# Kernel optimization log

Measured on AMD Instinct MI355X. Metric: run time of the kernel, lower is better.

Reference implementation:

```python
import jax, jax.numpy as jnp
import numpy as np

DIM = 1024
HEADS = 16
HEAD_DIM = DIM // HEADS
MLP_HIDDEN = DIM * 4
EPS = 1e-6


def _ln(x):
    # LayerNorm without affine, eps=1e-6
    mu = jnp.mean(x, axis=-1, keepdims=True)
    var = jnp.var(x, axis=-1, keepdims=True)
    return (x - mu) / jnp.sqrt(var + EPS)


def setup_inputs() -> dict:
    key = jax.random.key(0)
    ks = jax.random.split(key, 12)
    B, N = 8, 1024
    s = lambda fan: 1.0 / np.sqrt(fan)
    return {
        "x": jax.random.normal(ks[0], (B, N, DIM), jnp.float32),
        "c": jax.random.normal(ks[1], (B, DIM), jnp.float32),
        "w_qkv": jax.random.normal(ks[2], (DIM, 3 * DIM), jnp.float32) * s(DIM),
        "b_qkv": jnp.zeros((3 * DIM,), jnp.float32),
        "w_proj": jax.random.normal(ks[3], (DIM, DIM), jnp.float32) * s(DIM),
        "b_proj": jnp.zeros((DIM,), jnp.float32),
        "w_mlp1": jax.random.normal(ks[4], (DIM, MLP_HIDDEN), jnp.float32) * s(DIM),
        "b_mlp1": jnp.zeros((MLP_HIDDEN,), jnp.float32),
        "w_mlp2": jax.random.normal(ks[5], (MLP_HIDDEN, DIM), jnp.float32) * s(MLP_HIDDEN),
        "b_mlp2": jnp.zeros((DIM,), jnp.float32),
        "w_ada": jax.random.normal(ks[6], (DIM, 6 * DIM), jnp.float32) * s(DIM),
        "b_ada": jnp.zeros((6 * DIM,), jnp.float32),
    }


def _attention(h, w_qkv, b_qkv, w_proj, b_proj):
    B, N, C = h.shape
    qkv = h @ w_qkv + b_qkv  # [B,N,3C]
    qkv = qkv.reshape(B, N, 3, HEADS, HEAD_DIM)
    q, k, v = qkv[:, :, 0], qkv[:, :, 1], qkv[:, :, 2]  # [B,N,H,Dh]
    scale = HEAD_DIM ** -0.5
    attn = jnp.einsum("bqhd,bkhd->bhqk", q, k) * scale
    attn = jax.nn.softmax(attn, axis=-1)
    o = jnp.einsum("bhqk,bkhd->bqhd", attn, v).reshape(B, N, C)
    return o @ w_proj + b_proj


def reference(x, c, w_qkv, b_qkv, w_proj, b_proj, w_mlp1, b_mlp1, w_mlp2, b_mlp2, w_ada, b_ada):
    mod = (jax.nn.silu(c) @ w_ada + b_ada)[:, None, :]  # [B,1,6D]
    g1, be1, a1, g2, be2, a2 = jnp.split(mod, 6, axis=-1)
    h = _ln(x) * (1.0 + g1) + be1
    x = x + a1 * _attention(h, w_qkv, b_qkv, w_proj, b_proj)
    h = _ln(x) * (1.0 + g2) + be2
    mlp = jax.nn.gelu(h @ w_mlp1 + b_mlp1, approximate=False) @ w_mlp2 + b_mlp2
    return x + a2 * mlp
```

## Files before the change

kernel.cpp:

```cpp
#include <hip/hip_runtime.h>
#include <hip/hip_bf16.h>

#define DIMC 1024
#define SEQ  1024
#define NB   8
#define NH   16
#define HD2  64
#define EPSV 1e-6f

typedef short short8 __attribute__((ext_vector_type(8)));
typedef float floatx4 __attribute__((ext_vector_type(4)));

#define GLOAD_LDS(g, l) \
  __builtin_amdgcn_global_load_lds((const __attribute__((address_space(1))) unsigned int*)(g), \
                                   (__attribute__((address_space(3))) unsigned int*)(l), 16, 0, 0)

__device__ __forceinline__ float bf2f(unsigned short u){
  union { float f; unsigned int i; } v; v.i = ((unsigned int)u) << 16; return v.f;
}
__device__ __forceinline__ unsigned short f2bf(float f){
  union { float f; unsigned int i; } v; v.f = f;
  unsigned int r = v.i + 0x7fffu + ((v.i >> 16) & 1u);
  return (unsigned short)(r >> 16);
}

__global__ __launch_bounds__(256)
void tcvt_kernel(const float* __restrict__ in, unsigned short* __restrict__ out, int K, int N)
{
  __shared__ float tile[32][33];
  const int n0 = blockIdx.x * 32;
  const int k0 = blockIdx.y * 32;
  const int tx = threadIdx.x & 31;
  const int ty = threadIdx.x >> 5;
#pragma unroll
  for (int i = 0; i < 4; i++)
    tile[ty + i*8][tx] = in[(size_t)(k0 + ty + i*8) * N + n0 + tx];
  __syncthreads();
#pragma unroll
  for (int i = 0; i < 4; i++)
    out[(size_t)(n0 + ty + i*8) * K + k0 + tx] = f2bf(tile[tx][ty + i*8]);
}

__global__ __launch_bounds__(256)
void ada1_kernel(const float* __restrict__ c,
                 const float* __restrict__ w_ada,
                 float* __restrict__ partial)
{
  __shared__ float cs[NB][128];
  const int chunk = blockIdx.y;
  const int col = blockIdx.x * 256 + threadIdx.x;
  const int t = threadIdx.x;
  for (int i = t; i < NB * 128; i += 256) {
    const int b = i >> 7, k = i & 127;
    const float v = c[b * DIMC + chunk * 128 + k];
    cs[b][k] = v / (1.0f + __expf(-v));
  }
  __syncthreads();
  float acc[NB];
#pragma unroll
  for (int b = 0; b < NB; b++) acc[b] = 0.0f;
#pragma unroll 8
  for (int k = 0; k < 128; k++) {
    const float wv = w_ada[(size_t)(chunk * 128 + k) * 6144 + col];
#pragma unroll
    for (int b = 0; b < NB; b++) acc[b] = fmaf(cs[b][k], wv, acc[b]);
  }
#pragma unroll
  for (int b = 0; b < NB; b++)
    partial[((size_t)chunk * NB + b) * 6144 + col] = acc[b];
}

__global__ __launch_bounds__(256)
void ada2_kernel(const float* __restrict__ partial, const float* __restrict__ b_ada,
                 float* __restrict__ mod)
{
  const int i = blockIdx.x * 256 + threadIdx.x;
  const int b = i / 6144, col = i % 6144;
  float s = b_ada[col];
#pragma unroll
  for (int ch = 0; ch < 8; ch++) s += partial[((size_t)ch * NB + b) * 6144 + col];
  mod[i] = s;
}

__global__ __launch_bounds__(256)
void ln_kernel(const float* __restrict__ xin, const float* __restrict__ mod,
               int goff, int boff, unsigned short* __restrict__ hout)
{
  const int row = blockIdx.x;
  const int bb = row >> 10;
  const int t = threadIdx.x;
  const float4 x4 = *((const float4*)(xin + (size_t)row * DIMC) + t);
  const float v0 = x4.x, v1 = x4.y, v2 = x4.z, v3 = x4.w;
  float s  = v0 + v1 + v2 + v3;
  float ss = v0*v0 + v1*v1 + v2*v2 + v3*v3;
#pragma unroll
  for (int off = 32; off > 0; off >>= 1) {
    s  += __shfl_down(s,  off, 64);
    ss += __shfl_down(ss, off, 64);
  }
  __shared__ float red[10];
  const int w = t >> 6;
  if ((t & 63) == 0) { red[w] = s; red[4 + w] = ss; }
  __syncthreads();
  if (t == 0) {
    const float S  = red[0] + red[1] + red[2] + red[3];
    const float SS = red[4] + red[5] + red[6] + red[7];
    const float mu = S * (1.0f / 1024.0f);
    red[8] = mu;
    red[9] = rsqrtf(SS * (1.0f / 1024.0f) - mu * mu + EPSV);
  }
  __syncthreads();
  const float mu = red[8], rstd = red[9];
  const float* mrow = mod + (size_t)bb * 6144;
  const int d = t * 4;
  const float h0 = (v0 - mu) * rstd * (1.0f + mrow[goff + d + 0]) + mrow[boff + d + 0];
  const float h1 = (v1 - mu) * rstd * (1.0f + mrow[goff + d + 1]) + mrow[boff + d + 1];
  const float h2 = (v2 - mu) * rstd * (1.0f + mrow[goff + d + 2]) + mrow[boff + d + 2];
  const float h3 = (v3 - mu) * rstd * (1.0f + mrow[goff + d + 3]) + mrow[boff + d + 3];
  uint2 u;
  u.x = (unsigned)f2bf(h0) | ((unsigned)f2bf(h1) << 16);
  u.y = (unsigned)f2bf(h2) | ((unsigned)f2bf(h3) << 16);
  *((uint2*)(hout + (size_t)row * DIMC + d)) = u;
}

#define MF(a, b, c) __builtin_amdgcn_mfma_f32_16x16x32_bf16(a, b, c, 0, 0, 0)
#define FENCE() asm volatile("" ::: "memory")
#define BARRIER() do { FENCE(); __builtin_amdgcn_s_barrier(); FENCE(); } while (0)

template<int MODE>
__global__ __launch_bounds__(512, 2)
void gemm256_kernel(const unsigned short* __restrict__ A,
                    const unsigned short* __restrict__ Bt,
                    const float* __restrict__ bias,
                    void* __restrict__ Cout,
                    const float* __restrict__ resid,
                    const float* __restrict__ mod,
                    int M, int N, int K)
{
  __shared__ unsigned short As[2][16384];
  __shared__ unsigned short Bs[2][16384];

  const int mT = M >> 8;
  const int mb = mT >> 3;
  const int bid = blockIdx.x;
  const int xcd = bid & 7;
  const int local = bid >> 3;
  const int ni = local / mb;
  const int mi = xcd * mb + (local - ni * mb);
  const int m0 = mi << 8, n0 = ni << 8;

  const int tid = threadIdx.x;
  const int w = tid >> 6, lane = tid & 63;
  const int quad = lane >> 4, c16 = lane & 15;
  const int wm = w >> 2, wn = w & 3, w2 = w << 1;

  const int aRow = wm * 8192 + c16 * 64;
  const int bRow = (wn >> 1) * 8192 + ((wn & 1) * 64 + c16) * 64;
  const int sxz  = (c16 & 7) << 4;
  const int swz0 = ((0  + quad * 16) ^ sxz) >> 1;
  const int swz1 = ((64 + quad * 16) ^ sxz) >> 1;
#define LDA8(cc, i, SW) (*(const short8*)&As[cc][aRow + (i) * 1024 + (SW)])
#define LDB8(cc, j, SW) (*(const short8*)&Bs[cc][bRow + (j) * 1024 + (SW)])

  const int l8 = lane >> 3, lc = lane & 7;
  const int stC = ((lc ^ l8) << 3);
  const unsigned short* aSt = A  + (size_t)(m0 + w2 * 8 + l8) * K + stC;
  const unsigned short* bSt = Bt + (size_t)(n0 + w2 * 8 + l8) * K + stC;
#define STAGE_A(cc, h, kk0) do { \
  GLOAD_LDS(aSt + (size_t)((h) * 128    ) * K + (kk0), &As[cc][(h) * 8192 + w2 * 512      ]); \
  GLOAD_LDS(aSt + (size_t)((h) * 128 + 8) * K + (kk0), &As[cc][(h) * 8192 + w2 * 512 + 512]); \
} while (0)
#define STAGE_B(cc, h, kk0) do { \
  GLOAD_LDS(bSt + (size_t)((h) * 128    ) * K + (kk0), &Bs[cc][(h) * 8192 + w2 * 512      ]); \
  GLOAD_LDS(bSt + (size_t)((h) * 128 + 8) * K + (kk0), &Bs[cc][(h) * 8192 + w2 * 512 + 512]); \
} while (0)

  floatx4 acc[8][4];
#pragma unroll
  for (int i = 0; i < 8; i++)
#pragma unroll
    for (int j = 0; j < 4; j++) acc[i][j] = (floatx4)(0.0f);

#define MMROW(i, aE, aO) do { \
  acc[i][0] = MF(aE, bF00, acc[i][0]); acc[i][0] = MF(aO, bF01, acc[i][0]); \
  acc[i][1] = MF(aE, bF10, acc[i][1]); acc[i][1] = MF(aO, bF11, acc[i][1]); \
  acc[i][2] = MF(aE, bF20, acc[i][2]); acc[i][2] = MF(aO, bF21, acc[i][2]); \
  acc[i][3] = MF(aE, bF30, acc[i][3]); acc[i][3] = MF(aO, bF31, acc[i][3]); \
} while (0)

#define PH_TAIL(i0, i1) do { \
  BARRIER(); \
  asm volatile("s_waitcnt lgkmcnt(0)" ::: "memory"); \
  __builtin_amdgcn_s_setprio(1); \
  MMROW(i0, a0, a1); \
  MMROW(i1, a2, a3); \
  __builtin_amdgcn_s_setprio(0); \
} while (0)

#define GROUP(cc, oo, g) do { \
  const int kA_ = ((g) + 1) << 6; const int kB_ = ((g) + 2) << 6; \
  const bool dA_ = kA_ < K; const bool dB_ = kB_ < K; \
  short8 bF00 = LDB8(cc, 0, swz0), bF01 = LDB8(cc, 0, swz1); \
  short8 bF10 = LDB8(cc, 1, swz0), bF11 = LDB8(cc, 1, swz1); \
  short8 bF20 = LDB8(cc, 2, swz0), bF21 = LDB8(cc, 2, swz1); \
  short8 bF30 = LDB8(cc, 3, swz0), bF31 = LDB8(cc, 3, swz1); \
  short8 a0 = LDA8(cc, 0, swz0), a1 = LDA8(cc, 0, swz1); \
  short8 a2 = LDA8(cc, 1, swz0), a3 = LDA8(cc, 1, swz1); \
  if (dA_) STAGE_A(oo, 0, kA_); \
  PH_TAIL(0, 1); \
  BARRIER(); \
  a0 = LDA8(cc, 2, swz0); a1 = LDA8(cc, 2, swz1); \
  a2 = LDA8(cc, 3, swz0); a3 = LDA8(cc, 3, swz1); \
  if (dA_) STAGE_A(oo, 1, kA_); \
  PH_TAIL(2, 3); \
  BARRIER(); \
  a0 = LDA8(cc, 4, swz0); a1 = LDA8(cc, 4, swz1); \
  a2 = LDA8(cc, 5, swz0); a3 = LDA8(cc, 5, swz1); \
  if (dB_) STAGE_B(cc, 0, kB_); \
  PH_TAIL(4, 5); \
  BARRIER(); \
  a0 = LDA8(cc, 6, swz0); a1 = LDA8(cc, 6, swz1); \
  a2 = LDA8(cc, 7, swz0); a3 = LDA8(cc, 7, swz1); \
  if (dB_) STAGE_B(cc, 1, kB_); \
  PH_TAIL(6, 7); \
  if (dB_) { asm volatile("s_waitcnt vmcnt(4)" ::: "memory"); } \
  else     { asm volatile("s_waitcnt vmcnt(0)" ::: "memory"); } \
  BARRIER(); \
} while (0)

  STAGE_B(0, 0, 0);  STAGE_B(0, 1, 0);
  STAGE_A(0, 0, 0);  STAGE_A(0, 1, 0);
  STAGE_B(1, 0, 64); STAGE_B(1, 1, 64);
  asm volatile("s_waitcnt vmcnt(4)" ::: "memory");
  BARRIER();

  const int T = K >> 6;
  for (int g = 0; g < T; g += 2) {
    GROUP(0, 1, g);
    GROUP(1, 0, g + 1);
  }

  const int bb = m0 >> 10;
#pragma unroll
  for (int j = 0; j < 4; j++) {
    const int col = n0 + wn * 64 + j * 16 + c16;
    const float bv = bias[col];
    float av = 0.0f;
    if (MODE == 2) av = mod[(size_t)bb * 6144 + 2048 + col];
    if (MODE == 3) av = mod[(size_t)bb * 6144 + 5120 + col];
#pragma unroll
    for (int i = 0; i < 8; i++) {
      const int rowb = m0 + wm * 128 + i * 16 + quad * 4;
#pragma unroll
      for (int r = 0; r < 4; r++) {
        const int row = rowb + r;
        const size_t idx = (size_t)row * N + col;
        float v = acc[i][j][r] + bv;
        if (MODE == 0) {
          ((unsigned short*)Cout)[idx] = f2bf(v);
        } else if (MODE == 1) {
          v = 0.5f * v * (1.0f + erff(v * 0.70710678f));
          ((unsigned short*)Cout)[idx] = f2bf(v);
        } else {
          ((float*)Cout)[idx] = fmaf(av, v, resid[idx]);
        }
      }
    }
  }
#undef GROUP
#undef PH_TAIL
#undef MMROW
#undef STAGE_A
#undef STAGE_B
#undef LDA8
#undef LDB8
}

__global__ __launch_bounds__(256, 2)
void fattn_kernel(const unsigned short* __restrict__ qkv, unsigned short* __restrict__ o_out)
{
  __shared__ unsigned short Ks[64][72];
  __shared__ unsigned short Vt[64][72];
  __shared__ unsigned short Pt[4][32][72];

  const int blk = blockIdx.x;
  const int qt = blk & 7;
  const int h  = (blk >> 3) & 15;
  const int bb = blk >> 7;
  const int tid = threadIdx.x;
  const int w = tid >> 6;
  const int lane = tid & 63;
  const int quad = lane >> 4;
  const int c16 = lane & 15;
  const int q0 = qt * 128 + w * 32;

  short8 qf[2][2];
#pragma unroll
  for (int msub = 0; msub < 2; msub++)
#pragma unroll
    for (int kh = 0; kh < 2; kh++) {
      const size_t idx = ((size_t)((bb*SEQ + q0 + msub*16 + c16) * 3 + 0)) * DIMC
                       + h * HD2 + kh * 32 + quad * 8;
      const uint4 u = *(const uint4*)(qkv + idx);
      const unsigned short* pu = (const unsigned short*)&u;
      short8 r;
#pragma unroll
      for (int j = 0; j < 8; j++) r[j] = (short)f2bf(bf2f(pu[j]) * 0.125f);
      qf[msub][kh] = r;
    }

  floatx4 oacc[2][4];
  float lsum[2][4];
#pragma unroll
  for (int msub = 0; msub < 2; msub++) {
#pragma unroll
    for (int r = 0; r < 4; r++) lsum[msub][r] = 0.0f;
#pragma unroll
    for (int d = 0; d < 4; d++) oacc[msub][d] = (floatx4)(0.0f);
  }

  const int tok = tid & 63;
  const int dg = tid >> 6;

  for (int kt = 0; kt < 16; kt++) {
    __syncthreads();
    {
      const size_t base = ((size_t)((bb*SEQ + kt*64 + tok) * 3)) * DIMC + h * HD2 + dg * 16;
      const uint4 ku0 = *(const uint4*)(qkv + base + DIMC);
      const uint4 ku1 = *(const uint4*)(qkv + base + DIMC + 8);
      const uint4 vu0 = *(const uint4*)(qkv + base + 2*DIMC);
      const uint4 vu1 = *(const uint4*)(qkv + base + 2*DIMC + 8);
      *(uint4*)&Ks[tok][dg*16]     = ku0;
      *(uint4*)&Ks[tok][dg*16 + 8] = ku1;
      const unsigned short* vp0 = (const unsigned short*)&vu0;
      const unsigned short* vp1 = (const unsigned short*)&vu1;
#pragma unroll
      for (int j = 0; j < 8; j++) Vt[dg*16 + j][tok] = vp0[j];
#pragma unroll
      for (int j = 0; j < 8; j++) Vt[dg*16 + 8 + j][tok] = vp1[j];
    }
    __syncthreads();

    floatx4 s[2][4];
#pragma unroll
    for (int msub = 0; msub < 2; msub++)
#pragma unroll
      for (int nsub = 0; nsub < 4; nsub++) s[msub][nsub] = (floatx4)(0.0f);
#pragma unroll
    for (int nsub = 0; nsub < 4; nsub++) {
      const short8 kf0 = *(const short8*)&Ks[nsub*16 + c16][quad*8];
      const short8 kf1 = *(const short8*)&Ks[nsub*16 + c16][32 + quad*8];
#pragma unroll
      for (int msub = 0; msub < 2; msub++) {
        s[msub][nsub] = __builtin_amdgcn_mfma_f32_16x16x32_bf16(qf[msub][0], kf0, s[msub][nsub], 0, 0, 0);
        s[msub][nsub] = __builtin_amdgcn_mfma_f32_16x16x32_bf16(qf[msub][1], kf1, s[msub][nsub], 0, 0, 0);
      }
    }

#pragma unroll
    for (int msub = 0; msub < 2; msub++)
#pragma unroll
      for (int nsub = 0; nsub < 4; nsub++)
#pragma unroll
        for (int r = 0; r < 4; r++) {
          const float p = __expf(s[msub][nsub][r] - 8.0f);
          lsum[msub][r] += p;
          Pt[w][msub*16 + quad*4 + r][nsub*16 + c16] = f2bf(p);
        }

    short8 pa[2][2];
#pragma unroll
    for (int msub = 0; msub < 2; msub++) {
      pa[msub][0] = *(const short8*)&Pt[w][msub*16 + c16][quad*8];
      pa[msub][1] = *(const short8*)&Pt[w][msub*16 + c16][32 + quad*8];
    }
#pragma unroll
    for (int dsub = 0; dsub < 4; dsub++) {
      const short8 vf0 = *(const short8*)&Vt[dsub*16 + c16][quad*8];
      const short8 vf1 = *(const short8*)&Vt[dsub*16 + c16][32 + quad*8];
#pragma unroll
      for (int msub = 0; msub < 2; msub++) {
        oacc[msub][dsub] = __builtin_amdgcn_mfma_f32_16x16x32_bf16(pa[msub][0], vf0, oacc[msub][dsub], 0, 0, 0);
        oacc[msub][dsub] = __builtin_amdgcn_mfma_f32_16x16x32_bf16(pa[msub][1], vf1, oacc[msub][dsub], 0, 0, 0);
      }
    }
  }

#pragma unroll
  for (int msub = 0; msub < 2; msub++) {
    float rl[4];
#pragma unroll
    for (int r = 0; r < 4; r++) {
      float t = lsum[msub][r];
#pragma unroll
      for (int xm = 1; xm < 16; xm <<= 1) t += __shfl_xor(t, xm, 64);
      rl[r] = 1.0f / t;
    }
#pragma unroll
    for (int dsub = 0; dsub < 4; dsub++)
#pragma unroll
      for (int r = 0; r < 4; r++) {
        const size_t idx = (size_t)(bb*SEQ + q0 + msub*16 + quad*4 + r) * DIMC
                         + h * HD2 + dsub*16 + c16;
        o_out[idx] = f2bf(oacc[msub][dsub][r] * rl[r]);
      }
  }
}

extern "C" void kernel_launch(void* const* d_in, const int* in_sizes, int n_in,
                              void* d_out, int out_size, void* d_ws, size_t ws_size,
                              hipStream_t stream) {
  const float* x      = (const float*)d_in[0];
  const float* c      = (const float*)d_in[1];
  const float* w_qkv  = (const float*)d_in[2];
  const float* b_qkv  = (const float*)d_in[3];
  const float* w_proj = (const float*)d_in[4];
  const float* b_proj = (const float*)d_in[5];
  const float* w_mlp1 = (const float*)d_in[6];
  const float* b_mlp1 = (const float*)d_in[7];
  const float* w_mlp2 = (const float*)d_in[8];
  const float* b_mlp2 = (const float*)d_in[9];
  const float* w_ada  = (const float*)d_in[10];
  const float* b_ada  = (const float*)d_in[11];

  char* ws = (char*)d_ws;
  float*          mod     = (float*)(ws);
  unsigned short* wqkv_t  = (unsigned short*)(ws + 196608);
  unsigned short* wproj_t = (unsigned short*)(ws + 6488064);
  unsigned short* wmlp1_t = (unsigned short*)(ws + 8585216);
  unsigned short* wmlp2_t = (unsigned short*)(ws + 16973824);
  unsigned short* bufH    = (unsigned short*)(ws + 25362432);
  float*          adapart = (float*)(ws + 25362432);
  unsigned short* qkv     = (unsigned short*)(ws + 42139648);
  unsigned short* hid     = (unsigned short*)(ws + 42139648);
  float*          out     = (float*)d_out;

  const int M = NB * SEQ;

  tcvt_kernel<<<dim3(96, 32),  256, 0, stream>>>(w_qkv,  wqkv_t,  1024, 3072);
  tcvt_kernel<<<dim3(32, 32),  256, 0, stream>>>(w_proj, wproj_t, 1024, 1024);
  tcvt_kernel<<<dim3(128, 32), 256, 0, stream>>>(w_mlp1, wmlp1_t, 1024, 4096);
  tcvt_kernel<<<dim3(32, 128), 256, 0, stream>>>(w_mlp2, wmlp2_t, 4096, 1024);

  ada1_kernel<<<dim3(24, 8), 256, 0, stream>>>(c, w_ada, adapart);
  ada2_kernel<<<192, 256, 0, stream>>>(adapart, b_ada, mod);

  ln_kernel<<<M, 256, 0, stream>>>(x, mod, 0, 1024, bufH);
  gemm256_kernel<0><<<384, 512, 0, stream>>>(bufH, wqkv_t, b_qkv, qkv, nullptr, nullptr, M, 3072, 1024);
  fattn_kernel<<<1024, 256, 0, stream>>>(qkv, bufH);
  gemm256_kernel<2><<<128, 512, 0, stream>>>(bufH, wproj_t, b_proj, out, x, mod, M, 1024, 1024);
  ln_kernel<<<M, 256, 0, stream>>>(out, mod, 3072, 4096, bufH);

  const size_t fullHidEnd = 42139648ull + (size_t)M * 4096 * 2;
  if (ws_size >= fullHidEnd) {
    gemm256_kernel<1><<<512, 512, 0, stream>>>(bufH, wmlp1_t, b_mlp1, hid,
                                               nullptr, nullptr, M, 4096, 1024);
    gemm256_kernel<3><<<128, 512, 0, stream>>>(hid, wmlp2_t, b_mlp2, out,
                                               out, mod, M, 1024, 4096);
  } else {
    for (int half = 0; half < 2; half++) {
      const size_t roff = (size_t)half * 4096;
      gemm256_kernel<1><<<256, 512, 0, stream>>>(bufH + roff * DIMC, wmlp1_t, b_mlp1, hid,
                                                 nullptr, nullptr, 4096, 4096, 1024);
      gemm256_kernel<3><<<64, 512, 0, stream>>>(hid, wmlp2_t, b_mlp2, out + roff * DIMC,
                                                out + roff * DIMC, mod + (size_t)half * 4 * 6144,
                                                4096, 1024, 4096);
    }
  }
}
```

Measured before the change: 586.1 us.

## Add 256x128 GEMM tile variant, LDS-staged bf16 epilogue, and fast GELU

Templates the GEMM on the N tile width and adds a 256x128 variant with its own pipeline group. The QKV, proj and MLP2 GEMMs use it to launch more blocks (for example 128 to 256 for proj and MLP2) and fill the GPU better. Bf16 outputs are now staged through LDS so global stores are coalesced 16-byte writes instead of scattered 2-byte stores. The exact erff in the GELU epilogue is replaced by an Abramowitz-Stegun polynomial approximation, which trades a little accuracy for fewer instructions. The narrower tiles reuse each A tile less, so more global traffic per FLOP is possible.

```diff
diff --git a/kernel.cpp b/kernel.cpp
--- a/kernel.cpp
+++ b/kernel.cpp
@@ -22,6 +22,18 @@
   union { float f; unsigned int i; } v; v.f = f;
   unsigned int r = v.i + 0x7fffu + ((v.i >> 16) & 1u);
   return (unsigned short)(r >> 16);
+}
+
+__device__ __forceinline__ float gelu_f(float v){
+  const float z  = fabsf(v) * 0.70710678f;
+  const float t  = __builtin_amdgcn_rcpf(fmaf(0.3275911f, z, 1.0f));
+  float p = fmaf(t, 1.061405429f, -1.453152027f);
+  p = fmaf(t, p, 1.421413741f);
+  p = fmaf(t, p, -0.284496736f);
+  p = fmaf(t, p, 0.254829592f);
+  float erfz = fmaf(-p * t, __expf(-z * z), 1.0f);
+  erfz = (v < 0.0f) ? -erfz : erfz;
+  return 0.5f * v * (1.0f + erfz);
 }
 
 __global__ __launch_bounds__(256)
@@ -127,7 +139,7 @@
 #define FENCE() asm volatile("" ::: "memory")
 #define BARRIER() do { FENCE(); __builtin_amdgcn_s_barrier(); FENCE(); } while (0)
 
-template<int MODE>
+template<int MODE, int BN>
 __global__ __launch_bounds__(512, 2)
 void gemm256_kernel(const unsigned short* __restrict__ A,
                     const unsigned short* __restrict__ Bt,
@@ -137,8 +149,12 @@
                     const float* __restrict__ mod,
                     int M, int N, int K)
 {
+  constexpr int NWN = BN / 64;
+  constexpr int NWM = 8 / NWN;
+  constexpr int NI  = 256 / NWM / 16;
+
   __shared__ unsigned short As[2][16384];
-  __shared__ unsigned short Bs[2][16384];
+  __shared__ unsigned short Bs[2][BN * 64];
 
   const int mT = M >> 8;
   const int mb = mT >> 3;
@@ -147,15 +163,15 @@
   const int local = bid >> 3;
   const int ni = local / mb;
   const int mi = xcd * mb + (local - ni * mb);
-  const int m0 = mi << 8, n0 = ni << 8;
+  const int m0 = mi << 8, n0 = ni * BN;
 
   const int tid = threadIdx.x;
   const int w = tid >> 6, lane = tid & 63;
   const int quad = lane >> 4, c16 = lane & 15;
-  const int wm = w >> 2, wn = w & 3, w2 = w << 1;
-
-  const int aRow = wm * 8192 + c16 * 64;
-  const int bRow = (wn >> 1) * 8192 + ((wn & 1) * 64 + c16) * 64;
+  const int wm = w / NWN, wn = w % NWN, w2 = w << 1;
+
+  const int aRow = (wm * (NI * 16) + c16) * 64;
+  const int bRow = (wn * 64 + c16) * 64;
   const int sxz  = (c16 & 7) << 4;
   const int swz0 = ((0  + quad * 16) ^ sxz) >> 1;
   const int swz1 = ((64 + quad * 16) ^ sxz) >> 1;
@@ -175,9 +191,9 @@
   GLOAD_LDS(bSt + (size_t)((h) * 128 + 8) * K + (kk0), &Bs[cc][(h) * 8192 + w2 * 512 + 512]); \
 } while (0)
 
-  floatx4 acc[8][4];
-#pragma unroll
-  for (int i = 0; i < 8; i++)
+  floatx4 acc[NI][4];
+#pragma unroll
+  for (int i = 0; i < NI; i++)
 #pragma unroll
     for (int j = 0; j < 4; j++) acc[i][j] = (floatx4)(0.0f);
 
@@ -197,7 +213,7 @@
   __builtin_amdgcn_s_setprio(0); \
 } while (0)
 
-#define GROUP(cc, oo, g) do { \
+#define GROUP256(cc, oo, g) do { \
   const int kA_ = ((g) + 1) << 6; const int kB_ = ((g) + 2) << 6; \
   const bool dA_ = kA_ < K; const bool dB_ = kB_ < K; \
   short8 bF00 = LDB8(cc, 0, swz0), bF01 = LDB8(cc, 0, swz1); \
@@ -228,46 +244,93 @@
   BARRIER(); \
 } while (0)
 
-  STAGE_B(0, 0, 0);  STAGE_B(0, 1, 0);
-  STAGE_A(0, 0, 0);  STAGE_A(0, 1, 0);
-  STAGE_B(1, 0, 64); STAGE_B(1, 1, 64);
-  asm volatile("s_waitcnt vmcnt(4)" ::: "memory");
+#define GROUP128(cc, oo, g) do { \
+  const int kA_ = ((g) + 1) << 6; const int kB_ = ((g) + 2) << 6; \
+  const bool dA_ = kA_ < K; const bool dB_ = kB_ < K; \
+  short8 bF00 = LDB8(cc, 0, swz0), bF01 = LDB8(cc, 0, swz1); \
+  short8 bF10 = LDB8(cc, 1, swz0), bF11 = LDB8(cc, 1, swz1); \
+  short8 bF20 = LDB8(cc, 2, swz0), bF21 = LDB8(cc, 2, swz1); \
+  short8 bF30 = LDB8(cc, 3, swz0), bF31 = LDB8(cc, 3, swz1); \
+  short8 a0 = LDA8(cc, 0, swz0), a1 = LDA8(cc, 0, swz1); \
+  short8 a2 = LDA8(cc, 1, swz0), a3 = LDA8(cc, 1, swz1); \
+  if (dA_) { STAGE_A(oo, 0, kA_); STAGE_A(oo, 1, kA_); } \
+  PH_TAIL(0, 1); \
+  BARRIER(); \
+  a0 = LDA8(cc, 2, swz0); a1 = LDA8(cc, 2, swz1); \
+  a2 = LDA8(cc, 3, swz0); a3 = LDA8(cc, 3, swz1); \
+  if (dB_) STAGE_B(cc, 0, kB_); \
+  PH_TAIL(2, 3); \
+  if (dB_) { asm volatile("s_waitcnt vmcnt(2)" ::: "memory"); } \
+  else     { asm volatile("s_waitcnt vmcnt(0)" ::: "memory"); } \
+  BARRIER(); \
+} while (0)
+
+  if constexpr (BN == 256) {
+    STAGE_B(0, 0, 0);  STAGE_B(0, 1, 0);
+    STAGE_A(0, 0, 0);  STAGE_A(0, 1, 0);
+    STAGE_B(1, 0, 64); STAGE_B(1, 1, 64);
+    asm volatile("s_waitcnt vmcnt(4)" ::: "memory");
+  } else {
+    STAGE_B(0, 0, 0);
+    STAGE_A(0, 0, 0);  STAGE_A(0, 1, 0);
+    STAGE_B(1, 0, 64);
+    asm volatile("s_waitcnt vmcnt(2)" ::: "memory");
+  }
   BARRIER();
 
   const int T = K >> 6;
   for (int g = 0; g < T; g += 2) {
-    GROUP(0, 1, g);
-    GROUP(1, 0, g + 1);
+    if constexpr (BN == 256) { GROUP256(0, 1, g); GROUP256(1, 0, g + 1); }
+    else                     { GROUP128(0, 1, g); GROUP128(1, 0, g + 1); }
   }
 
   const int bb = m0 >> 10;
-#pragma unroll
-  for (int j = 0; j < 4; j++) {
-    const int col = n0 + wn * 64 + j * 16 + c16;
-    const float bv = bias[col];
-    float av = 0.0f;
-    if (MODE == 2) av = mod[(size_t)bb * 6144 + 2048 + col];
-    if (MODE == 3) av = mod[(size_t)bb * 6144 + 5120 + col];
-#pragma unroll
-    for (int i = 0; i < 8; i++) {
-      const int rowb = m0 + wm * 128 + i * 16 + quad * 4;
-#pragma unroll
-      for (int r = 0; r < 4; r++) {
-        const int row = rowb + r;
-        const size_t idx = (size_t)row * N + col;
-        float v = acc[i][j][r] + bv;
-        if (MODE == 0) {
-          ((unsigned short*)Cout)[idx] = f2bf(v);
-        } else if (MODE == 1) {
-          v = 0.5f * v * (1.0f + erff(v * 0.70710678f));
-          ((unsigned short*)Cout)[idx] = f2bf(v);
-        } else {
-          ((float*)Cout)[idx] = fmaf(av, v, resid[idx]);
+  if (MODE == 0 || MODE == 1) {
+    unsigned short* eb;
+    if constexpr (BN == 256)
+      eb = (w < 4 ? (unsigned short*)As : (unsigned short*)Bs) + (w & 3) * 8192;
+    else
+      eb = (unsigned short*)As + w * (NI * 1024);
+#pragma unroll
+    for (int j = 0; j < 4; j++) {
+      const int col = n0 + wn * 64 + j * 16 + c16;
+      const float bv = bias[col];
+#pragma unroll
+      for (int i = 0; i < NI; i++)
+#pragma unroll
+        for (int r = 0; r < 4; r++) {
+          float v = acc[i][j][r] + bv;
+          if (MODE == 1) v = gelu_f(v);
+          eb[(i * 16 + quad * 4 + r) * 64 + j * 16 + c16] = f2bf(v);
+        }
+    }
+    unsigned short* cw = (unsigned short*)Cout
+                       + (size_t)(m0 + wm * (NI * 16)) * N + n0 + wn * 64;
+    const int seg = lane & 7;
+#pragma unroll
+    for (int it = 0; it < NI * 2; it++) {
+      const int row = it * 8 + (lane >> 3);
+      *(uint4*)(cw + (size_t)row * N + seg * 8) = *(const uint4*)&eb[row * 64 + seg * 8];
+    }
+  } else {
+#pragma unroll
+    for (int j = 0; j < 4; j++) {
+      const int col = n0 + wn * 64 + j * 16 + c16;
+      const float bv = bias[col];
+      const float av = mod[(size_t)bb * 6144 + (MODE == 2 ? 2048 : 5120) + col];
+#pragma unroll
+      for (int i = 0; i < NI; i++) {
+        const int rowb = m0 + wm * (NI * 16) + i * 16 + quad * 4;
+#pragma unroll
+        for (int r = 0; r < 4; r++) {
+          const size_t idx = (size_t)(rowb + r) * N + col;
+          ((float*)Cout)[idx] = fmaf(av, acc[i][j][r] + bv, resid[idx]);
         }
       }
     }
   }
-#undef GROUP
+#undef GROUP256
+#undef GROUP128
 #undef PH_TAIL
 #undef MMROW
 #undef STAGE_A
@@ -446,25 +509,25 @@
   ada2_kernel<<<192, 256, 0, stream>>>(adapart, b_ada, mod);
 
   ln_kernel<<<M, 256, 0, stream>>>(x, mod, 0, 1024, bufH);
-  gemm256_kernel<0><<<384, 512, 0, stream>>>(bufH, wqkv_t, b_qkv, qkv, nullptr, nullptr, M, 3072, 1024);
+  gemm256_kernel<0,128><<<768, 512, 0, stream>>>(bufH, wqkv_t, b_qkv, qkv, nullptr, nullptr, M, 3072, 1024);
   fattn_kernel<<<1024, 256, 0, stream>>>(qkv, bufH);
-  gemm256_kernel<2><<<128, 512, 0, stream>>>(bufH, wproj_t, b_proj, out, x, mod, M, 1024, 1024);
+  gemm256_kernel<2,128><<<256, 512, 0, stream>>>(bufH, wproj_t, b_proj, out, x, mod, M, 1024, 1024);
   ln_kernel<<<M, 256, 0, stream>>>(out, mod, 3072, 4096, bufH);
 
   const size_t fullHidEnd = 42139648ull + (size_t)M * 4096 * 2;
   if (ws_size >= fullHidEnd) {
-    gemm256_kernel<1><<<512, 512, 0, stream>>>(bufH, wmlp1_t, b_mlp1, hid,
-                                               nullptr, nullptr, M, 4096, 1024);
-    gemm256_kernel<3><<<128, 512, 0, stream>>>(hid, wmlp2_t, b_mlp2, out,
-                                               out, mod, M, 1024, 4096);
+    gemm256_kernel<1,256><<<512, 512, 0, stream>>>(bufH, wmlp1_t, b_mlp1, hid,
+                                                   nullptr, nullptr, M, 4096, 1024);
+    gemm256_kernel<3,128><<<256, 512, 0, stream>>>(hid, wmlp2_t, b_mlp2, out,
+                                                   out, mod, M, 1024, 4096);
   } else {
     for (int half = 0; half < 2; half++) {
       const size_t roff = (size_t)half * 4096;
-      gemm256_kernel<1><<<256, 512, 0, stream>>>(bufH + roff * DIMC, wmlp1_t, b_mlp1, hid,
-                                                 nullptr, nullptr, 4096, 4096, 1024);
-      gemm256_kernel<3><<<64, 512, 0, stream>>>(hid, wmlp2_t, b_mlp2, out + roff * DIMC,
-                                                out + roff * DIMC, mod + (size_t)half * 4 * 6144,
-                                                4096, 1024, 4096);
-    }
-  }
-}
+      gemm256_kernel<1,256><<<256, 512, 0, stream>>>(bufH + roff * DIMC, wmlp1_t, b_mlp1, hid,
+                                                     nullptr, nullptr, 4096, 4096, 1024);
+      gemm256_kernel<3,128><<<128, 512, 0, stream>>>(hid, wmlp2_t, b_mlp2, out + roff * DIMC,
+                                                     out + roff * DIMC, mod + (size_t)half * 4 * 6144,
+                                                     4096, 1024, 4096);
+    }
+  }
+}
```

After: 494.1 us. 1.19x faster.
